# Optimization experiments

Hardware: AMD Instinct MI355X
Metric: run time of the kernel (lower is better)

Reference implementation:

```python
import jax, jax.numpy as jnp
import numpy as np

N_HEAD = 16
N_EMBD = 1024
B, T = 2, 2048


def setup_inputs() -> dict:
    key = jax.random.key(0)
    ks = jax.random.split(key, 5)
    C = N_EMBD
    x = jax.random.normal(ks[0], (B, T, C), dtype=jnp.float32)
    # nn.Linear default init scale ~ 1/sqrt(fan_in); use small normal for numerics
    s = 1.0 / np.sqrt(C)
    W_attn = jax.random.normal(ks[1], (C, 3 * C), dtype=jnp.float32) * s
    b_attn = jax.random.normal(ks[2], (3 * C,), dtype=jnp.float32) * s
    W_proj = jax.random.normal(ks[3], (C, C), dtype=jnp.float32) * s
    b_proj = jax.random.normal(ks[4], (C,), dtype=jnp.float32) * s
    return {"x": x, "W_attn": W_attn, "b_attn": b_attn, "W_proj": W_proj, "b_proj": b_proj}


def reference(x, W_attn, b_attn, W_proj, b_proj):
    Bs, Ts, C = x.shape
    H = N_HEAD
    D = C // H  # head dim
    qkv = x @ W_attn + b_attn  # [B, T, 3C]
    q, k, v = jnp.split(qkv, 3, axis=2)
    # [B, T, H, D] -> [B, H, T, D]
    q = q.reshape(Bs, Ts, H, D).transpose(0, 2, 1, 3)
    k = k.reshape(Bs, Ts, H, D).transpose(0, 2, 1, 3)
    v = v.reshape(Bs, Ts, H, D).transpose(0, 2, 1, 3)
    scale = 1.0 / jnp.sqrt(jnp.asarray(D, dtype=x.dtype))
    att = jnp.einsum("bhqd,bhkd->bhqk", q, k) * scale  # [B, H, T, T]
    causal = jnp.tril(jnp.ones((Ts, Ts), dtype=bool))
    att = jnp.where(causal, att, -jnp.inf)
    att = jax.nn.softmax(att, axis=-1)
    y = jnp.einsum("bhqk,bhkd->bhqd", att, v)  # [B, H, T, D]
    y = y.transpose(0, 2, 1, 3).reshape(Bs, Ts, C)
    return y @ W_proj + b_proj
```

## Files before the change

kernel.cpp:

```cpp
#include <hip/hip_runtime.h>
#include <stdint.h>

typedef unsigned short u16;
typedef __attribute__((ext_vector_type(8))) short bf16x8;
typedef __attribute__((ext_vector_type(4))) float f32x4;
typedef __attribute__((ext_vector_type(4))) int   i32x4;
typedef __attribute__((ext_vector_type(4))) unsigned short u16x4;

#define MFMA16(a, b, c) __builtin_amdgcn_mfma_f32_16x16x32_bf16((a), (b), (c), 0, 0, 0)

#define BATCH 2
#define TSEQ  2048
#define CEMB  1024
#define NHEAD 16
#define DHEAD 64
#define BHTOT 32
#define MROWS 4096

__device__ __forceinline__ u16 bf16r(float f) {
  uint32_t u = __builtin_bit_cast(uint32_t, f);
  u += 0x7fffu + ((u >> 16) & 1u);
  return (u16)(u >> 16);
}

__device__ __forceinline__ float bf2f(short v) {
  return __builtin_bit_cast(float, ((uint32_t)(u16)v) << 16);
}

__device__ __forceinline__ bf16x8 scale8(bf16x8 a, float s) {
  bf16x8 r;
#pragma unroll
  for (int i = 0; i < 8; i++) r[i] = (short)bf16r(bf2f(a[i]) * s);
  return r;
}

__device__ __forceinline__ void gl2lds16(const void* g, void* l) {
  __builtin_amdgcn_global_load_lds(
      (const __attribute__((address_space(1))) uint32_t*)g,
      (__attribute__((address_space(3))) uint32_t*)l, 16, 0, 0);
}

__global__ void conv_x(const float* __restrict__ x, u16* __restrict__ xb, int n) {
  int i = (blockIdx.x * blockDim.x + threadIdx.x) * 4;
  if (i < n) {
    f32x4 v = *(const f32x4*)(x + i);
    u16x4 o;
    o[0] = bf16r(v[0]); o[1] = bf16r(v[1]); o[2] = bf16r(v[2]); o[3] = bf16r(v[3]);
    *(u16x4*)(xb + i) = o;
  }
}

__global__ void transpose_w(const float* __restrict__ W, u16* __restrict__ WT, int K, int N) {
  __shared__ float t[32][33];
  int k0 = blockIdx.y * 32, n0 = blockIdx.x * 32;
  int tx = threadIdx.x & 31, ty = threadIdx.x >> 5;
  for (int i = 0; i < 4; i++)
    t[ty + i * 8][tx] = W[(size_t)(k0 + ty + i * 8) * N + n0 + tx];
  __syncthreads();
  for (int i = 0; i < 4; i++)
    WT[(size_t)(n0 + ty + i * 8) * K + k0 + tx] = bf16r(t[tx][ty + i * 8]);
}

__device__ __forceinline__ void gemm_mainloop(const u16* __restrict__ A,
                                              const u16* __restrict__ Bt,
                                              int K, int m0, int n0,
                                              u16* AsU, u16* BsU, f32x4 acc[4][4]) {
  const int tid = threadIdx.x;
  const int wv = tid >> 6, ln = tid & 63;
  const int lr = ln & 15, lg = ln >> 4;
  const int wr = (wv >> 1) * 64, wc = (wv & 1) * 64;

  for (int mi = 0; mi < 4; mi++)
    for (int ni = 0; ni < 4; ni++) acc[mi][ni] = f32x4{0.f, 0.f, 0.f, 0.f};

  for (int k0 = 0; k0 < K; k0 += 32) {
    for (int p = 0; p < 2; ++p) {
      int chunk = p * 256 + tid;
      int row = chunk >> 2;
      int c8  = (chunk & 3) << 3;
      u16* abase = AsU + (size_t)(p * 256 + wv * 64) * 8;
      u16* bbase = BsU + (size_t)(p * 256 + wv * 64) * 8;
      gl2lds16(A  + (size_t)(m0 + row) * K + k0 + c8, abase);
      gl2lds16(Bt + (size_t)(n0 + row) * K + k0 + c8, bbase);
    }
    __syncthreads();
    bf16x8 af[4], bf[4];
    for (int mi = 0; mi < 4; mi++)
      af[mi] = *(const bf16x8*)&AsU[(size_t)(wr + mi * 16 + lr) * 32 + lg * 8];
    for (int ni = 0; ni < 4; ni++)
      bf[ni] = *(const bf16x8*)&BsU[(size_t)(wc + ni * 16 + lr) * 32 + lg * 8];
    for (int mi = 0; mi < 4; mi++)
      for (int ni = 0; ni < 4; ni++)
        acc[mi][ni] = MFMA16(af[mi], bf[ni], acc[mi][ni]);
    __syncthreads();
  }
}

__global__ __launch_bounds__(256, 2) void qkv_gemm(const u16* __restrict__ xb,
                                                   const u16* __restrict__ WaT,
                                                   const float* __restrict__ b_attn,
                                                   u16* __restrict__ qb, u16* __restrict__ kb,
                                                   u16* __restrict__ vT) {
  __shared__ u16 AsU[128 * 32];
  __shared__ u16 BsU[128 * 32];
  const int m0 = blockIdx.y * 128, n0 = blockIdx.x * 128;
  f32x4 acc[4][4];
  gemm_mainloop(xb, WaT, CEMB, m0, n0, AsU, BsU, acc);

  const int tid = threadIdx.x;
  const int wv = tid >> 6, ln = tid & 63, lr = ln & 15, lg = ln >> 4;
  const int wr = (wv >> 1) * 64, wc = (wv & 1) * 64;
  for (int mi = 0; mi < 4; mi++)
    for (int ni = 0; ni < 4; ni++) {
      int col = n0 + wc + ni * 16 + lr;
      float bias = b_attn[col];
      int which = col >> 10;
      int cl = col & 1023, h = cl >> 6, d = cl & 63;
      for (int j = 0; j < 4; j++) {
        int m = m0 + wr + mi * 16 + lg * 4 + j;
        int b = m >> 11, t = m & 2047;
        u16 bv = bf16r(acc[mi][ni][j] + bias);
        size_t bh = (size_t)(b * NHEAD + h);
        if (which == 0)      qb[(bh * TSEQ + t) * DHEAD + d] = bv;
        else if (which == 1) kb[(bh * TSEQ + t) * DHEAD + d] = bv;
        else                 vT[(bh * DHEAD + d) * TSEQ + t] = bv;
      }
    }
}

__global__ __launch_bounds__(256, 2) void attn(const u16* __restrict__ qb,
                                               const u16* __restrict__ kb,
                                               const u16* __restrict__ vT,
                                               u16* __restrict__ yb) {
  const int flat = blockIdx.x;
  const int x = flat & 7;
  const int l = flat >> 3;
  int bh, qblk;
  if (l < 32) { bh = 4 * x + (l >> 3); qblk = 15 - (l & 7); }
  else        { int l2 = l - 32; bh = 4 * x + (l2 >> 3); qblk = l2 & 7; }
  const int tid = threadIdx.x, wv = tid >> 6, ln = tid & 63, lr = ln & 15, lg = ln >> 4;

  __shared__ u16 Ks[2][64][72];
  __shared__ u16 Vs[2][64][72];
  __shared__ u16 Ps[4][2][16][72];

  const int wq0 = qblk * 128 + wv * 32;
  const float SCL = 0.125f * 1.44269504f;

  bf16x8 qf[2][2];
#pragma unroll
  for (int qs = 0; qs < 2; qs++) {
    const u16* qrow = qb + ((size_t)bh * TSEQ + (wq0 + qs * 16 + lr)) * DHEAD + lg * 8;
    qf[qs][0] = scale8(*(const bf16x8*)(qrow), SCL);
    qf[qs][1] = scale8(*(const bf16x8*)(qrow + 32), SCL);
  }

  f32x4 acc[2][4];
#pragma unroll
  for (int qs = 0; qs < 2; qs++)
#pragma unroll
    for (int df = 0; df < 4; df++) acc[qs][df] = f32x4{0.f, 0.f, 0.f, 0.f};
  float mrun[2] = {-1e30f, -1e30f}, lrun[2] = {0.f, 0.f};

  const int ntiles = 2 * qblk + 2;
  const int srow = tid >> 3, sc8 = (tid & 7) << 3;

  i32x4 kreg[2], vreg[2];
#pragma unroll
  for (int p = 0; p < 2; p++) {
    int row = p * 32 + srow;
    i32x4 k0 = *(const i32x4*)(kb + ((size_t)bh * TSEQ + row) * DHEAD + sc8);
    i32x4 v0 = *(const i32x4*)(vT + ((size_t)bh * DHEAD + row) * TSEQ + sc8);
    *(i32x4*)&Ks[0][row][sc8] = k0;
    *(i32x4*)&Vs[0][row][sc8] = v0;
  }
#pragma unroll
  for (int p = 0; p < 2; p++) {
    int row = p * 32 + srow;
    kreg[p] = *(const i32x4*)(kb + ((size_t)bh * TSEQ + 64 + row) * DHEAD + sc8);
    vreg[p] = *(const i32x4*)(vT + ((size_t)bh * DHEAD + row) * TSEQ + 64 + sc8);
  }

  int c = 0;
  for (int kt = 0; kt < ntiles; kt++) {
    const int kbase = kt * 64;
    __syncthreads();

    f32x4 s[2][4];
#pragma unroll
    for (int st = 0; st < 4; st++) {
      bf16x8 kf0 = *(const bf16x8*)&Ks[c][st * 16 + lr][lg * 8];
      bf16x8 kf1 = *(const bf16x8*)&Ks[c][st * 16 + lr][32 + lg * 8];
#pragma unroll
      for (int qs = 0; qs < 2; qs++) {
        f32x4 z = f32x4{0.f, 0.f, 0.f, 0.f};
        z = MFMA16(kf0, qf[qs][0], z);
        z = MFMA16(kf1, qf[qs][1], z);
        s[qs][st] = z;
      }
    }

    if (kt + 1 < ntiles) {
#pragma unroll
      for (int p = 0; p < 2; p++) {
        int row = p * 32 + srow;
        *(i32x4*)&Ks[c ^ 1][row][sc8] = kreg[p];
        *(i32x4*)&Vs[c ^ 1][row][sc8] = vreg[p];
      }
    }
    if (kt + 2 < ntiles) {
      const int nb = kbase + 128;
#pragma unroll
      for (int p = 0; p < 2; p++) {
        int row = p * 32 + srow;
        kreg[p] = *(const i32x4*)(kb + ((size_t)bh * TSEQ + nb + row) * DHEAD + sc8);
        vreg[p] = *(const i32x4*)(vT + ((size_t)bh * DHEAD + row) * TSEQ + nb + sc8);
      }
    }

#pragma unroll
    for (int qs = 0; qs < 2; qs++) {
      const int qgmin = wq0 + qs * 16;
      float mt = -1e30f;
      if (kbase + 63 <= qgmin) {
#pragma unroll
        for (int st = 0; st < 4; st++)
#pragma unroll
          for (int j = 0; j < 4; j++) mt = fmaxf(mt, s[qs][st][j]);
      } else {
        const int qg = qgmin + lr;
#pragma unroll
        for (int st = 0; st < 4; st++)
#pragma unroll
          for (int j = 0; j < 4; j++) {
            int kg = kbase + st * 16 + lg * 4 + j;
            float v = (kg <= qg) ? s[qs][st][j] : -1e30f;
            s[qs][st][j] = v;
            mt = fmaxf(mt, v);
          }
      }
      mt = fmaxf(mt, __shfl_xor(mt, 16));
      mt = fmaxf(mt, __shfl_xor(mt, 32));
      if (!__all(mt <= mrun[qs])) {
        float mnew = fmaxf(mrun[qs], mt);
        float al = __builtin_amdgcn_exp2f(mrun[qs] - mnew);
#pragma unroll
        for (int df = 0; df < 4; df++)
#pragma unroll
          for (int j = 0; j < 4; j++) acc[qs][df][j] *= al;
        lrun[qs] *= al;
        mrun[qs] = mnew;
      }
      float rs = 0.f;
#pragma unroll
      for (int st = 0; st < 4; st++)
#pragma unroll
        for (int j = 0; j < 4; j++) {
          float p = __builtin_amdgcn_exp2f(s[qs][st][j] - mrun[qs]);
          s[qs][st][j] = p;
          rs += p;
        }
      rs += __shfl_xor(rs, 16);
      rs += __shfl_xor(rs, 32);
      lrun[qs] += rs;
#pragma unroll
      for (int st = 0; st < 4; st++) {
        uint32_t w0 = (uint32_t)bf16r(s[qs][st][0]) | ((uint32_t)bf16r(s[qs][st][1]) << 16);
        uint32_t w1 = (uint32_t)bf16r(s[qs][st][2]) | ((uint32_t)bf16r(s[qs][st][3]) << 16);
        *(uint32_t*)&Ps[wv][qs][lr][st * 16 + lg * 4]     = w0;
        *(uint32_t*)&Ps[wv][qs][lr][st * 16 + lg * 4 + 2] = w1;
      }
    }
    __asm__ volatile("s_waitcnt lgkmcnt(0)" ::: "memory");
    __builtin_amdgcn_sched_barrier(0);

    bf16x8 pf[2][2];
#pragma unroll
    for (int qs = 0; qs < 2; qs++)
#pragma unroll
      for (int ks = 0; ks < 2; ks++)
        pf[qs][ks] = *(const bf16x8*)&Ps[wv][qs][lr][ks * 32 + lg * 8];
#pragma unroll
    for (int df = 0; df < 4; df++)
#pragma unroll
      for (int ks = 0; ks < 2; ks++) {
        bf16x8 vf = *(const bf16x8*)&Vs[c][df * 16 + lr][ks * 32 + lg * 8];
        acc[0][df] = MFMA16(vf, pf[0][ks], acc[0][df]);
        acc[1][df] = MFMA16(vf, pf[1][ks], acc[1][df]);
      }
    c ^= 1;
  }

  const int b = bh >> 4, h = bh & 15;
#pragma unroll
  for (int qs = 0; qs < 2; qs++) {
    float inv = 1.f / lrun[qs];
    int tg = wq0 + qs * 16 + lr;
#pragma unroll
    for (int df = 0; df < 4; df++) {
      u16x4 o;
#pragma unroll
      for (int j = 0; j < 4; j++) o[j] = bf16r(acc[qs][df][j] * inv);
      *(u16x4*)&yb[((size_t)b * TSEQ + tg) * CEMB + h * 64 + df * 16 + lg * 4] = o;
    }
  }
}

__global__ __launch_bounds__(256, 2) void proj_gemm(const u16* __restrict__ yb,
                                                    const u16* __restrict__ WpT,
                                                    const float* __restrict__ b_proj,
                                                    float* __restrict__ out) {
  __shared__ u16 AsU[128 * 32];
  __shared__ u16 BsU[128 * 32];
  const int m0 = blockIdx.y * 128, n0 = blockIdx.x * 128;
  f32x4 acc[4][4];
  gemm_mainloop(yb, WpT, CEMB, m0, n0, AsU, BsU, acc);

  const int tid = threadIdx.x;
  const int wv = tid >> 6, ln = tid & 63, lr = ln & 15, lg = ln >> 4;
  const int wr = (wv >> 1) * 64, wc = (wv & 1) * 64;
  for (int mi = 0; mi < 4; mi++)
    for (int ni = 0; ni < 4; ni++) {
      int col = n0 + wc + ni * 16 + lr;
      float bias = b_proj[col];
      for (int j = 0; j < 4; j++) {
        int m = m0 + wr + mi * 16 + lg * 4 + j;
        out[(size_t)m * CEMB + col] = acc[mi][ni][j] + bias;
      }
    }
}

extern "C" void kernel_launch(void* const* d_in, const int* in_sizes, int n_in,
                              void* d_out, int out_size, void* d_ws, size_t ws_size,
                              hipStream_t stream) {
  const float* x      = (const float*)d_in[0];
  const float* W_attn = (const float*)d_in[1];
  const float* b_attn = (const float*)d_in[2];
  const float* W_proj = (const float*)d_in[3];
  const float* b_proj = (const float*)d_in[4];
  float* out = (float*)d_out;
  char* ws = (char*)d_ws;

  u16* xb  = (u16*)(ws);
  u16* WaT = (u16*)(ws + 8388608);
  u16* WpT = (u16*)(ws + 14680064);
  u16* qb  = (u16*)(ws + 16777216);
  u16* kb  = (u16*)(ws + 25165824);
  u16* vT  = (u16*)(ws + 33554432);
  u16* yb  = (u16*)(ws + 41943040);

  hipLaunchKernelGGL(conv_x, dim3(4096), dim3(256), 0, stream, x, xb, MROWS * CEMB);
  hipLaunchKernelGGL(transpose_w, dim3(96, 32), dim3(256), 0, stream, W_attn, WaT, 1024, 3072);
  hipLaunchKernelGGL(transpose_w, dim3(32, 32), dim3(256), 0, stream, W_proj, WpT, 1024, 1024);
  hipLaunchKernelGGL(qkv_gemm, dim3(24, 32), dim3(256), 0, stream, xb, WaT, b_attn, qb, kb, vT);
  hipLaunchKernelGGL(attn, dim3(512), dim3(256), 0, stream, qb, kb, vT, yb);
  hipLaunchKernelGGL(proj_gemm, dim3(8, 32), dim3(256), 0, stream, yb, WpT, b_proj, out);
}
```

Measured before the change: 202.6 us.

## Halve attention query tile, double grid, pass P via lane shuffles not LDS

Result: faster. 189.9 us (-6.3%).

```diff
diff --git a/kernel.cpp b/kernel.cpp
--- a/kernel.cpp
+++ b/kernel.cpp
@@ -5,6 +5,7 @@
 typedef __attribute__((ext_vector_type(8))) short bf16x8;
 typedef __attribute__((ext_vector_type(4))) float f32x4;
 typedef __attribute__((ext_vector_type(4))) int   i32x4;
+typedef __attribute__((ext_vector_type(4))) unsigned int u32x4;
 typedef __attribute__((ext_vector_type(4))) unsigned short u16x4;
 
 #define MFMA16(a, b, c) __builtin_amdgcn_mfma_f32_16x16x32_bf16((a), (b), (c), 0, 0, 0)
@@ -128,51 +129,47 @@
     }
 }
 
-__global__ __launch_bounds__(256, 2) void attn(const u16* __restrict__ qb,
+__global__ __launch_bounds__(256, 4) void attn(const u16* __restrict__ qb,
                                                const u16* __restrict__ kb,
                                                const u16* __restrict__ vT,
                                                u16* __restrict__ yb) {
   const int flat = blockIdx.x;
   const int x = flat & 7;
   const int l = flat >> 3;
-  int bh, qblk;
-  if (l < 32) { bh = 4 * x + (l >> 3); qblk = 15 - (l & 7); }
-  else        { int l2 = l - 32; bh = 4 * x + (l2 >> 3); qblk = l2 & 7; }
+  const int r = l & 31, a = l >> 5, rq = r & 7;
+  const int bh = 4 * x + (r >> 3);
+  const int qblk = (a == 0) ? 31 - rq : (a == 1) ? rq : (a == 2) ? 23 - rq : 8 + rq;
+
   const int tid = threadIdx.x, wv = tid >> 6, ln = tid & 63, lr = ln & 15, lg = ln >> 4;
+  const int b1 = lg >> 1, b0 = lg & 1;
 
   __shared__ u16 Ks[2][64][72];
   __shared__ u16 Vs[2][64][72];
-  __shared__ u16 Ps[4][2][16][72];
-
-  const int wq0 = qblk * 128 + wv * 32;
+
+  const int wq0 = qblk * 64 + wv * 16;
   const float SCL = 0.125f * 1.44269504f;
 
-  bf16x8 qf[2][2];
-#pragma unroll
-  for (int qs = 0; qs < 2; qs++) {
-    const u16* qrow = qb + ((size_t)bh * TSEQ + (wq0 + qs * 16 + lr)) * DHEAD + lg * 8;
-    qf[qs][0] = scale8(*(const bf16x8*)(qrow), SCL);
-    qf[qs][1] = scale8(*(const bf16x8*)(qrow + 32), SCL);
-  }
-
-  f32x4 acc[2][4];
-#pragma unroll
-  for (int qs = 0; qs < 2; qs++)
-#pragma unroll
-    for (int df = 0; df < 4; df++) acc[qs][df] = f32x4{0.f, 0.f, 0.f, 0.f};
-  float mrun[2] = {-1e30f, -1e30f}, lrun[2] = {0.f, 0.f};
-
-  const int ntiles = 2 * qblk + 2;
+  bf16x8 qf0, qf1;
+  {
+    const u16* qrow = qb + ((size_t)bh * TSEQ + (wq0 + lr)) * DHEAD + lg * 8;
+    qf0 = scale8(*(const bf16x8*)(qrow), SCL);
+    qf1 = scale8(*(const bf16x8*)(qrow + 32), SCL);
+  }
+
+  f32x4 acc[4];
+#pragma unroll
+  for (int df = 0; df < 4; df++) acc[df] = f32x4{0.f, 0.f, 0.f, 0.f};
+  float mrun = -1e30f, lrun = 0.f;
+
+  const int ntiles = qblk + 1;
   const int srow = tid >> 3, sc8 = (tid & 7) << 3;
 
   i32x4 kreg[2], vreg[2];
 #pragma unroll
   for (int p = 0; p < 2; p++) {
     int row = p * 32 + srow;
-    i32x4 k0 = *(const i32x4*)(kb + ((size_t)bh * TSEQ + row) * DHEAD + sc8);
-    i32x4 v0 = *(const i32x4*)(vT + ((size_t)bh * DHEAD + row) * TSEQ + sc8);
-    *(i32x4*)&Ks[0][row][sc8] = k0;
-    *(i32x4*)&Vs[0][row][sc8] = v0;
+    *(i32x4*)&Ks[0][row][sc8] = *(const i32x4*)(kb + ((size_t)bh * TSEQ + row) * DHEAD + sc8);
+    *(i32x4*)&Vs[0][row][sc8] = *(const i32x4*)(vT + ((size_t)bh * DHEAD + row) * TSEQ + sc8);
   }
 #pragma unroll
   for (int p = 0; p < 2; p++) {
@@ -186,18 +183,15 @@
     const int kbase = kt * 64;
     __syncthreads();
 
-    f32x4 s[2][4];
+    f32x4 s[4];
 #pragma unroll
     for (int st = 0; st < 4; st++) {
       bf16x8 kf0 = *(const bf16x8*)&Ks[c][st * 16 + lr][lg * 8];
       bf16x8 kf1 = *(const bf16x8*)&Ks[c][st * 16 + lr][32 + lg * 8];
-#pragma unroll
-      for (int qs = 0; qs < 2; qs++) {
-        f32x4 z = f32x4{0.f, 0.f, 0.f, 0.f};
-        z = MFMA16(kf0, qf[qs][0], z);
-        z = MFMA16(kf1, qf[qs][1], z);
-        s[qs][st] = z;
-      }
+      f32x4 z = f32x4{0.f, 0.f, 0.f, 0.f};
+      z = MFMA16(kf0, qf0, z);
+      z = MFMA16(kf1, qf1, z);
+      s[st] = z;
     }
 
     if (kt + 1 < ntiles) {
@@ -218,91 +212,103 @@
       }
     }
 
-#pragma unroll
-    for (int qs = 0; qs < 2; qs++) {
-      const int qgmin = wq0 + qs * 16;
-      float mt = -1e30f;
-      if (kbase + 63 <= qgmin) {
-#pragma unroll
-        for (int st = 0; st < 4; st++)
-#pragma unroll
-          for (int j = 0; j < 4; j++) mt = fmaxf(mt, s[qs][st][j]);
-      } else {
-        const int qg = qgmin + lr;
-#pragma unroll
-        for (int st = 0; st < 4; st++)
-#pragma unroll
-          for (int j = 0; j < 4; j++) {
-            int kg = kbase + st * 16 + lg * 4 + j;
-            float v = (kg <= qg) ? s[qs][st][j] : -1e30f;
-            s[qs][st][j] = v;
-            mt = fmaxf(mt, v);
-          }
-      }
-      mt = fmaxf(mt, __shfl_xor(mt, 16));
-      mt = fmaxf(mt, __shfl_xor(mt, 32));
-      if (!__all(mt <= mrun[qs])) {
-        float mnew = fmaxf(mrun[qs], mt);
-        float al = __builtin_amdgcn_exp2f(mrun[qs] - mnew);
-#pragma unroll
-        for (int df = 0; df < 4; df++)
-#pragma unroll
-          for (int j = 0; j < 4; j++) acc[qs][df][j] *= al;
-        lrun[qs] *= al;
-        mrun[qs] = mnew;
-      }
-      float rs = 0.f;
+    float mt = -1e30f;
+    if (kt == ntiles - 1) {
+      const int qg = wq0 + lr;
 #pragma unroll
       for (int st = 0; st < 4; st++)
 #pragma unroll
         for (int j = 0; j < 4; j++) {
-          float p = __builtin_amdgcn_exp2f(s[qs][st][j] - mrun[qs]);
-          s[qs][st][j] = p;
-          rs += p;
+          int kg = kbase + st * 16 + lg * 4 + j;
+          float v = (kg <= qg) ? s[st][j] : -1e30f;
+          s[st][j] = v;
+          mt = fmaxf(mt, v);
         }
-      rs += __shfl_xor(rs, 16);
-      rs += __shfl_xor(rs, 32);
-      lrun[qs] += rs;
-#pragma unroll
-      for (int st = 0; st < 4; st++) {
-        uint32_t w0 = (uint32_t)bf16r(s[qs][st][0]) | ((uint32_t)bf16r(s[qs][st][1]) << 16);
-        uint32_t w1 = (uint32_t)bf16r(s[qs][st][2]) | ((uint32_t)bf16r(s[qs][st][3]) << 16);
-        *(uint32_t*)&Ps[wv][qs][lr][st * 16 + lg * 4]     = w0;
-        *(uint32_t*)&Ps[wv][qs][lr][st * 16 + lg * 4 + 2] = w1;
-      }
-    }
-    __asm__ volatile("s_waitcnt lgkmcnt(0)" ::: "memory");
-    __builtin_amdgcn_sched_barrier(0);
-
-    bf16x8 pf[2][2];
-#pragma unroll
-    for (int qs = 0; qs < 2; qs++)
-#pragma unroll
-      for (int ks = 0; ks < 2; ks++)
-        pf[qs][ks] = *(const bf16x8*)&Ps[wv][qs][lr][ks * 32 + lg * 8];
-#pragma unroll
-    for (int df = 0; df < 4; df++)
-#pragma unroll
-      for (int ks = 0; ks < 2; ks++) {
-        bf16x8 vf = *(const bf16x8*)&Vs[c][df * 16 + lr][ks * 32 + lg * 8];
-        acc[0][df] = MFMA16(vf, pf[0][ks], acc[0][df]);
-        acc[1][df] = MFMA16(vf, pf[1][ks], acc[1][df]);
-      }
+    } else {
+#pragma unroll
+      for (int st = 0; st < 4; st++)
+#pragma unroll
+        for (int j = 0; j < 4; j++) mt = fmaxf(mt, s[st][j]);
+    }
+    mt = fmaxf(mt, __shfl_xor(mt, 16));
+    mt = fmaxf(mt, __shfl_xor(mt, 32));
+    if (!__all(mt <= mrun)) {
+      float mnew = fmaxf(mrun, mt);
+      float al = __builtin_amdgcn_exp2f(mrun - mnew);
+#pragma unroll
+      for (int df = 0; df < 4; df++)
+#pragma unroll
+        for (int j = 0; j < 4; j++) acc[df][j] *= al;
+      lrun *= al;
+      mrun = mnew;
+    }
+    float rs = 0.f;
+#pragma unroll
+    for (int st = 0; st < 4; st++)
+#pragma unroll
+      for (int j = 0; j < 4; j++) {
+        float p = __builtin_amdgcn_exp2f(s[st][j] - mrun);
+        s[st][j] = p;
+        rs += p;
+      }
+    rs += __shfl_xor(rs, 16);
+    rs += __shfl_xor(rs, 32);
+    lrun += rs;
+
+    uint32_t W[4][2];
+#pragma unroll
+    for (int st = 0; st < 4; st++) {
+      W[st][0] = (uint32_t)bf16r(s[st][0]) | ((uint32_t)bf16r(s[st][1]) << 16);
+      W[st][1] = (uint32_t)bf16r(s[st][2]) | ((uint32_t)bf16r(s[st][3]) << 16);
+    }
+    uint32_t Ka[2], Kb[2], Xa[2], Xb[2];
+#pragma unroll
+    for (int h = 0; h < 2; h++) {
+      uint32_t S1a = b1 ? W[0][h] : W[1][h];
+      uint32_t S1b = b1 ? W[2][h] : W[3][h];
+      Xa[h] = __shfl_xor(S1a, 32);
+      Xb[h] = __shfl_xor(S1b, 32);
+      Ka[h] = b1 ? W[1][h] : W[0][h];
+      Kb[h] = b1 ? W[3][h] : W[2][h];
+    }
+    const bool e = (b0 == b1);
+    uint32_t Ta[2], Tb[2], Ra[2], Rb[2];
+#pragma unroll
+    for (int h = 0; h < 2; h++) {
+      uint32_t Cah = e ? Xa[h] : Ka[h];
+      uint32_t Cbh = e ? Xb[h] : Kb[h];
+      Ta[h] = e ? Ka[h] : Xa[h];
+      Tb[h] = e ? Kb[h] : Xb[h];
+      Ra[h] = __shfl_xor(Cah, 16);
+      Rb[h] = __shfl_xor(Cbh, 16);
+    }
+    u32x4 w0, w1;
+    w0[0] = b0 ? Ra[0] : Ta[0];  w0[1] = b0 ? Ra[1] : Ta[1];
+    w0[2] = b0 ? Ta[0] : Ra[0];  w0[3] = b0 ? Ta[1] : Ra[1];
+    w1[0] = b0 ? Rb[0] : Tb[0];  w1[1] = b0 ? Rb[1] : Tb[1];
+    w1[2] = b0 ? Tb[0] : Rb[0];  w1[3] = b0 ? Tb[1] : Rb[1];
+    bf16x8 pf0 = __builtin_bit_cast(bf16x8, w0);
+    bf16x8 pf1 = __builtin_bit_cast(bf16x8, w1);
+
+#pragma unroll
+    for (int df = 0; df < 4; df++) {
+      bf16x8 vf0 = *(const bf16x8*)&Vs[c][df * 16 + lr][lg * 8];
+      bf16x8 vf1 = *(const bf16x8*)&Vs[c][df * 16 + lr][32 + lg * 8];
+      acc[df] = MFMA16(vf0, pf0, acc[df]);
+      acc[df] = MFMA16(vf1, pf1, acc[df]);
+    }
     c ^= 1;
   }
 
   const int b = bh >> 4, h = bh & 15;
-#pragma unroll
-  for (int qs = 0; qs < 2; qs++) {
-    float inv = 1.f / lrun[qs];
-    int tg = wq0 + qs * 16 + lr;
-#pragma unroll
-    for (int df = 0; df < 4; df++) {
-      u16x4 o;
-#pragma unroll
-      for (int j = 0; j < 4; j++) o[j] = bf16r(acc[qs][df][j] * inv);
-      *(u16x4*)&yb[((size_t)b * TSEQ + tg) * CEMB + h * 64 + df * 16 + lg * 4] = o;
-    }
+  float inv = 1.f / lrun;
+  int tg = wq0 + lr;
+#pragma unroll
+  for (int df = 0; df < 4; df++) {
+    u16x4 o;
+#pragma unroll
+    for (int j = 0; j < 4; j++) o[j] = bf16r(acc[df][j] * inv);
+    *(u16x4*)&yb[((size_t)b * TSEQ + tg) * CEMB + h * 64 + df * 16 + lg * 4] = o;
   }
 }
 
@@ -353,6 +359,6 @@
   hipLaunchKernelGGL(transpose_w, dim3(96, 32), dim3(256), 0, stream, W_attn, WaT, 1024, 3072);
   hipLaunchKernelGGL(transpose_w, dim3(32, 32), dim3(256), 0, stream, W_proj, WpT, 1024, 1024);
   hipLaunchKernelGGL(qkv_gemm, dim3(24, 32), dim3(256), 0, stream, xb, WaT, b_attn, qb, kb, vT);
-  hipLaunchKernelGGL(attn, dim3(512), dim3(256), 0, stream, qb, kb, vT, yb);
+  hipLaunchKernelGGL(attn, dim3(1024), dim3(256), 0, stream, qb, kb, vT, yb);
   hipLaunchKernelGGL(proj_gemm, dim3(8, 32), dim3(256), 0, stream, yb, WpT, b_proj, out);
 }
```
